# Optimization experiments

Hardware: AMD Instinct MI355X
Metric: run time of the kernel (lower is better)

## Reference

```python
import jax, jax.numpy as jnp
import numpy as np

B, DIM, S, CS, H = 1024, 64, 256, 500, 128

def setup_inputs() -> dict:
    key = jax.random.key(0)
    ks = jax.random.split(key, 16)
    def rn(k, shape, scale=0.05):
        return jax.random.normal(k, shape, dtype=jnp.float32) * scale
    return {
        "x": rn(ks[0], (B, DIM, S - 1), 1.0),
        "snippet": jax.random.randint(ks[1], (B, DIM), 0, CS, dtype=jnp.int64),
        "snippet_list": rn(ks[2], (DIM, CS, S), 1.0),
        "W_ih": rn(ks[3], (3 * H, 2 * DIM)),
        "W_hh": rn(ks[4], (3 * H, H)),
        "b_ih": rn(ks[5], (3 * H,)),
        "b_hh": rn(ks[6], (3 * H,)),
        "W1": rn(ks[7], (H // 2, H)),
        "b1": rn(ks[8], (H // 2,)),
        "W2": rn(ks[9], (H // 4, H // 2)),
        "b2": rn(ks[10], (H // 4,)),
        "W3": rn(ks[11], (H // 8, H // 4)),
        "b3": rn(ks[12], (H // 8,)),
        "W_last": rn(ks[13], (DIM, H // 8 + DIM)),
        "b_last": rn(ks[14], (DIM,)),
    }

def _leaky(v):
    return jax.nn.leaky_relu(v, negative_slope=0.01)

def _gru_last(x_seq, W_ih, W_hh, b_ih, b_hh):
    # x_seq: [B, T, I]; returns last hidden state [B, H]
    xg = jnp.einsum('bti,gi->btg', x_seq, W_ih) + b_ih  # [B, T, 3H]
    h0 = jnp.zeros((x_seq.shape[0], H), dtype=x_seq.dtype)
    def step(h, xg_t):
        hg = h @ W_hh.T + b_hh
        xr, xz, xn = jnp.split(xg_t, 3, axis=-1)
        hr, hz, hn = jnp.split(hg, 3, axis=-1)
        r = jax.nn.sigmoid(xr + hr)
        z = jax.nn.sigmoid(xz + hz)
        n = jnp.tanh(xn + r * hn)
        h_new = (1.0 - z) * n + z * h
        return h_new, None
    h_last, _ = jax.lax.scan(step, h0, jnp.swapaxes(xg, 0, 1))
    return h_last

def reference(x, snippet, snippet_list, W_ih, W_hh, b_ih, b_hh,
              W1, b1, W2, b2, W3, b3, W_last, b_last):
    # vectorized gather: snip[b, d, :] = snippet_list[d, snippet[b, d], :]
    snip = snippet_list[jnp.arange(DIM)[None, :], snippet]  # [B, DIM, S]
    last = snip[:, :, -1]          # [B, DIM]
    snip = snip[:, :, :-1]         # [B, DIM, S-1]
    xc = jnp.concatenate((x, snip), axis=1)       # [B, 2*DIM, S-1]
    xc = jnp.swapaxes(xc, 1, 2)                   # [B, S-1, 2*DIM]
    h = _gru_last(xc, W_ih, W_hh, b_ih, b_hh)     # [B, H]
    h = _leaky(h @ W1.T + b1)
    h = _leaky(h @ W2.T + b2)
    h = _leaky(h @ W3.T + b3)
    h = jnp.concatenate((h, last), axis=1)        # [B, H//8 + DIM]
    out = _leaky(h @ W_last.T + b_last)           # [B, DIM]
    return out
```

## Files before the change

kernel.cpp:

```cpp
#include <hip/hip_runtime.h>
#include <hip/hip_bf16.h>

#define B_    1024
#define DIMC  64
#define T_    255
#define H_    128
#define CS_   500
#define S_    256

#define MROWS 16
#define NBLK  (B_ / MROWS)
#define NTHR  512
#define TCH   16
#define XSTR  136

typedef __attribute__((ext_vector_type(8))) short bf16x8;
typedef __attribute__((ext_vector_type(4))) float f32x4;
typedef __attribute__((ext_vector_type(4))) float fv4;

__device__ __forceinline__ unsigned short f2bf(float f) {
    unsigned int u = __builtin_bit_cast(unsigned int, f);
    return (unsigned short)((u + 0x7FFFu + ((u >> 16) & 1u)) >> 16);
}
__device__ __forceinline__ float fast_rcp(float x) { return __builtin_amdgcn_rcpf(x); }
__device__ __forceinline__ float sigm(float x)   { float e = __expf(-x); return fast_rcp(1.0f + e); }
__device__ __forceinline__ float tanh_f(float x) { float e = __expf(2.0f * x); return 1.0f - 2.0f * fast_rcp(1.0f + e); }
__device__ __forceinline__ float leaky(float x)  { return x > 0.0f ? x : 0.01f * x; }
__device__ __forceinline__ int   imin(int a, int b) { return a < b ? a : b; }

#define OW1 0
#define OW2 8256
#define OW3 10336
#define OWL 10864
#define OHF 16048
#define OS1 18096
#define OS2 18608
#define OS3 18864
#define OSL 18992

__global__ __launch_bounds__(NTHR, 2)
void gru_fused(const float* __restrict__ x, const int* __restrict__ snippet,
               const float* __restrict__ slist,
               const float* __restrict__ W_ih, const float* __restrict__ W_hh,
               const float* __restrict__ b_ih, const float* __restrict__ b_hh,
               const float* __restrict__ W1, const float* __restrict__ b1,
               const float* __restrict__ W2, const float* __restrict__ b2,
               const float* __restrict__ W3, const float* __restrict__ b3,
               const float* __restrict__ Wl, const float* __restrict__ bl,
               float* __restrict__ out)
{
    __shared__ __attribute__((aligned(16))) unsigned short sh_x[2][TCH * MROWS * XSTR];
    __shared__ __attribute__((aligned(16))) unsigned short sh_h[2][MROWS * XSTR];
    __shared__ int sh_idx[MROWS * DIMC];

    const int tid   = threadIdx.x;
    const int bbase = blockIdx.x * MROWS;
    const int lane  = tid & 63;
    const int wv    = tid >> 6;
    const int l15   = lane & 15;
    const int l4    = lane >> 4;

    for (int i = tid; i < MROWS * DIMC; i += NTHR) {
        int r = i >> 6, d = i & 63;
        sh_idx[i] = snippet[(bbase + r) * DIMC + d];
    }
    for (int i = tid; i < MROWS * XSTR; i += NTHR) sh_h[0][i] = 0;

    bf16x8 wih[3][4], whh[3][4];
    {
        const int g = (wv << 4) + l15;
#pragma unroll
        for (int gt = 0; gt < 3; ++gt) {
#pragma unroll
            for (int kb = 0; kb < 4; ++kb) {
                const float* p1 = W_ih + (size_t)(gt * 128 + g) * 128 + kb * 32 + (l4 << 3);
                const float* p2 = W_hh + (size_t)(gt * 128 + g) * 128 + kb * 32 + (l4 << 3);
                bf16x8 a, b;
#pragma unroll
                for (int e = 0; e < 8; ++e) { a[e] = (short)f2bf(p1[e]); b[e] = (short)f2bf(p2[e]); }
                wih[gt][kb] = a; whh[gt][kb] = b;
            }
        }
    }
    const int jj = (wv << 4) + l15;
    const float bias_r = b_ih[jj]       + b_hh[jj];
    const float bias_z = b_ih[128 + jj] + b_hh[128 + jj];
    const float bxn    = b_ih[256 + jj];
    const float bhn    = b_hh[256 + jj];

    __syncthreads();

    int rowu[2], k0u[2], isx[2];
    const float* pa[2]; const float* pb[2];
#pragma unroll
    for (int un = 0; un < 2; ++un) {
        int u  = tid + un * NTHR;
        int r  = u >> 6;
        int k0 = (u & 63) << 1;
        rowu[un] = r; k0u[un] = k0;
        if (k0 < DIMC) {
            isx[un] = 1;
            pa[un] = x + ((size_t)(bbase + r) * DIMC + k0) * T_;
            pb[un] = pa[un] + T_;
        } else {
            isx[un] = 0;
            int d = k0 - DIMC;
            pa[un] = slist + ((size_t)d       * CS_ + sh_idx[(r << 6) + d])     * S_;
            pb[un] = slist + ((size_t)(d + 1) * CS_ + sh_idx[(r << 6) + d + 1]) * S_;
        }
    }

    fv4 sa[2][4], sb[2][4];

    auto issue = [&](int t0) {
#pragma unroll
        for (int un = 0; un < 2; ++un) {
#pragma unroll
            for (int g = 0; g < 4; ++g) {
                int off = t0 + g * 4;
                if (isx[un] && off + 3 > T_ - 1) {
                    fv4 va, vb;
#pragma unroll
                    for (int e = 0; e < 4; ++e) {
                        int tt = imin(off + e, T_ - 1);
                        va[e] = pa[un][tt]; vb[e] = pb[un][tt];
                    }
                    sa[un][g] = va; sb[un][g] = vb;
                } else {
                    fv4 va, vb;
                    __builtin_memcpy(&va, pa[un] + off, 16);
                    __builtin_memcpy(&vb, pb[un] + off, 16);
                    sa[un][g] = va; sb[un][g] = vb;
                }
            }
        }
    };

    auto commit = [&](int buf) {
#pragma unroll
        for (int un = 0; un < 2; ++un) {
#pragma unroll
            for (int g = 0; g < 4; ++g) {
#pragma unroll
                for (int e = 0; e < 4; ++e) {
                    int t = g * 4 + e;
                    unsigned pk = (unsigned)f2bf(sa[un][g][e]) | ((unsigned)f2bf(sb[un][g][e]) << 16);
                    *(unsigned*)&sh_x[buf][(t * MROWS + rowu[un]) * XSTR + k0u[un]] = pk;
                }
            }
        }
    };

    int cur = 0;
    float hprev[4] = {0.f, 0.f, 0.f, 0.f};

    auto step = [&](int bx, int t) {
        const unsigned short* xp = &sh_x[bx][(t * MROWS + l15) * XSTR + (l4 << 3)];
        const unsigned short* hp = &sh_h[cur][l15 * XSTR + (l4 << 3)];
        bf16x8 axv[4], ahv[4];
#pragma unroll
        for (int kb = 0; kb < 4; ++kb) {
            axv[kb] = *(const bf16x8*)(xp + kb * 32);
            ahv[kb] = *(const bf16x8*)(hp + kb * 32);
        }
        f32x4 ar = {0.f, 0.f, 0.f, 0.f}, az = ar, axn = ar, ahn = ar;
#pragma unroll
        for (int kb = 0; kb < 4; ++kb) {
            ar  = __builtin_amdgcn_mfma_f32_16x16x32_bf16(axv[kb], wih[0][kb], ar,  0, 0, 0);
            az  = __builtin_amdgcn_mfma_f32_16x16x32_bf16(axv[kb], wih[1][kb], az,  0, 0, 0);
            axn = __builtin_amdgcn_mfma_f32_16x16x32_bf16(axv[kb], wih[2][kb], axn, 0, 0, 0);
            ar  = __builtin_amdgcn_mfma_f32_16x16x32_bf16(ahv[kb], whh[0][kb], ar,  0, 0, 0);
            az  = __builtin_amdgcn_mfma_f32_16x16x32_bf16(ahv[kb], whh[1][kb], az,  0, 0, 0);
            ahn = __builtin_amdgcn_mfma_f32_16x16x32_bf16(ahv[kb], whh[2][kb], ahn, 0, 0, 0);
        }
#pragma unroll
        for (int q = 0; q < 4; ++q) {
            float r = sigm(ar[q] + bias_r);
            float z = sigm(az[q] + bias_z);
            float n = tanh_f(axn[q] + bxn + r * (ahn[q] + bhn));
            float hn = (1.0f - z) * n + z * hprev[q];
            hprev[q] = hn;
            sh_h[cur ^ 1][((l4 << 2) + q) * XSTR + jj] = f2bf(hn);
        }
        __syncthreads();
        cur ^= 1;
    };

    issue(0);
    commit(0);
    __syncthreads();

    for (int c = 0; c < 15; ++c) {
        issue((c + 1) * TCH);
        for (int t = 0; t < TCH; ++t) step(c & 1, t);
        commit((c + 1) & 1);
        __syncthreads();
    }
    for (int t = 0; t < 15; ++t) step(1, t);

    float* wl = (float*)sh_x;

    for (int i = tid; i < 8192; i += NTHR) wl[OW1 + (i >> 7) * 129 + (i & 127)] = W1[i];
    for (int i = tid; i < 2048; i += NTHR) wl[OW2 + (i >> 6) * 65  + (i & 63)]  = W2[i];
    for (int i = tid; i < 512;  i += NTHR) wl[OW3 + (i >> 5) * 33  + (i & 31)]  = W3[i];
    for (int i = tid; i < 5120; i += NTHR) wl[OWL + (i / 80) * 81  + (i % 80)]  = Wl[i];
#pragma unroll
    for (int q = 0; q < 4; ++q) wl[OHF + ((l4 << 2) + q) * 128 + jj] = hprev[q];
    __syncthreads();

    for (int mloc = 0; mloc < 2; ++mloc) {
        const int m = (wv << 1) + mloc;
        {
            float s = b1[lane];
            const float* w = wl + OW1 + lane * 129;
            for (int k = 0; k < 128; ++k) s += wl[OHF + m * 128 + k] * w[k];
            wl[OS1 + wv * 64 + lane] = leaky(s);
        }
        __syncthreads();
        if (lane < 32) {
            float s = b2[lane];
            const float* w = wl + OW2 + lane * 65;
            for (int k = 0; k < 64; ++k) s += wl[OS1 + wv * 64 + k] * w[k];
            wl[OS2 + wv * 32 + lane] = leaky(s);
        } else {
            int d = lane - 32;
            wl[OSL + wv * 64 + d]      = slist[((size_t)d        * CS_ + sh_idx[(m << 6) + d])      * S_ + (S_ - 1)];
            wl[OSL + wv * 64 + d + 32] = slist[((size_t)(d + 32) * CS_ + sh_idx[(m << 6) + d + 32]) * S_ + (S_ - 1)];
        }
        __syncthreads();
        if (lane < 16) {
            float s = b3[lane];
            const float* w = wl + OW3 + lane * 33;
            for (int k = 0; k < 32; ++k) s += wl[OS2 + wv * 32 + k] * w[k];
            wl[OS3 + wv * 16 + lane] = leaky(s);
        }
        __syncthreads();
        {
            float s = bl[lane];
            const float* w = wl + OWL + lane * 81;
#pragma unroll
            for (int i = 0; i < 16; ++i) s += wl[OS3 + wv * 16 + i] * w[i];
            for (int d = 0; d < 64; ++d) s += wl[OSL + wv * 64 + d] * w[16 + d];
            out[(size_t)(bbase + m) * DIMC + lane] = leaky(s);
        }
        __syncthreads();
    }
}

extern "C" void kernel_launch(void* const* d_in, const int* in_sizes, int n_in,
                              void* d_out, int out_size, void* d_ws, size_t ws_size,
                              hipStream_t stream) {
    (void)in_sizes; (void)n_in; (void)out_size; (void)d_ws; (void)ws_size;
    const float* x       = (const float*)d_in[0];
    const int*   snippet = (const int*)  d_in[1];
    const float* slist   = (const float*)d_in[2];
    const float* W_ih    = (const float*)d_in[3];
    const float* W_hh    = (const float*)d_in[4];
    const float* b_ih    = (const float*)d_in[5];
    const float* b_hh    = (const float*)d_in[6];
    const float* W1      = (const float*)d_in[7];
    const float* b1      = (const float*)d_in[8];
    const float* W2      = (const float*)d_in[9];
    const float* b2      = (const float*)d_in[10];
    const float* W3      = (const float*)d_in[11];
    const float* b3      = (const float*)d_in[12];
    const float* Wl      = (const float*)d_in[13];
    const float* bl      = (const float*)d_in[14];
    float* out = (float*)d_out;

    hipLaunchKernelGGL(gru_fused, dim3(NBLK), dim3(NTHR), 0, stream,
                       x, snippet, slist, W_ih, W_hh, b_ih, b_hh,
                       W1, b1, W2, b2, W3, b3, Wl, bl, out);
}
```

Baseline: 308.5 us.

## Split GRU step into batched input-gate MFMAs and a shortened recurrent chain

The input-projection MFMAs are now computed four timesteps at a time, separately from the serial recurrence. Each step's recurrent chain then runs only the hidden-state MFMAs, split into two independent accumulator chains so more of them can be in flight. The time chunk shrinks from 16 to 8 steps, shared memory is packed into one manually laid-out buffer, per-step barriers become a raw lgkmcnt wait plus s_barrier, and weight loads use 16-byte vectors. This shortens the latency-bound critical path per timestep, at the cost of more chunk-level syncs and hand-computed shared-memory offsets.

```diff
diff --git a/kernel.cpp b/kernel.cpp
--- a/kernel.cpp
+++ b/kernel.cpp
@@ -11,12 +11,15 @@
 #define MROWS 16
 #define NBLK  (B_ / MROWS)
 #define NTHR  512
-#define TCH   16
+#define TCH   8
 #define XSTR  136
+
+#define OFF_H   69632
+#define OFF_IDX 78336
+#define SMEMB   82432
 
 typedef __attribute__((ext_vector_type(8))) short bf16x8;
 typedef __attribute__((ext_vector_type(4))) float f32x4;
-typedef __attribute__((ext_vector_type(4))) float fv4;
 
 __device__ __forceinline__ unsigned short f2bf(float f) {
     unsigned int u = __builtin_bit_cast(unsigned int, f);
@@ -27,6 +30,9 @@
 __device__ __forceinline__ float tanh_f(float x) { float e = __expf(2.0f * x); return 1.0f - 2.0f * fast_rcp(1.0f + e); }
 __device__ __forceinline__ float leaky(float x)  { return x > 0.0f ? x : 0.01f * x; }
 __device__ __forceinline__ int   imin(int a, int b) { return a < b ? a : b; }
+__device__ __forceinline__ void bar_lgkm() {
+    asm volatile("s_waitcnt lgkmcnt(0)\n\ts_barrier" ::: "memory");
+}
 
 #define OW1 0
 #define OW2 8256
@@ -49,9 +55,10 @@
                const float* __restrict__ Wl, const float* __restrict__ bl,
                float* __restrict__ out)
 {
-    __shared__ __attribute__((aligned(16))) unsigned short sh_x[2][TCH * MROWS * XSTR];
-    __shared__ __attribute__((aligned(16))) unsigned short sh_h[2][MROWS * XSTR];
-    __shared__ int sh_idx[MROWS * DIMC];
+    __shared__ __attribute__((aligned(16))) unsigned char smem[SMEMB];
+    unsigned short* shx0 = (unsigned short*)smem;
+    unsigned short* shh0 = (unsigned short*)(smem + OFF_H);
+    int*            sidx = (int*)(smem + OFF_IDX);
 
     const int tid   = threadIdx.x;
     const int bbase = blockIdx.x * MROWS;
@@ -62,9 +69,9 @@
 
     for (int i = tid; i < MROWS * DIMC; i += NTHR) {
         int r = i >> 6, d = i & 63;
-        sh_idx[i] = snippet[(bbase + r) * DIMC + d];
-    }
-    for (int i = tid; i < MROWS * XSTR; i += NTHR) sh_h[0][i] = 0;
+        sidx[i] = snippet[(bbase + r) * DIMC + d];
+    }
+    for (int i = tid; i < MROWS * XSTR; i += NTHR) shh0[i] = 0;
 
     bf16x8 wih[3][4], whh[3][4];
     {
@@ -75,10 +82,16 @@
             for (int kb = 0; kb < 4; ++kb) {
                 const float* p1 = W_ih + (size_t)(gt * 128 + g) * 128 + kb * 32 + (l4 << 3);
                 const float* p2 = W_hh + (size_t)(gt * 128 + g) * 128 + kb * 32 + (l4 << 3);
-                bf16x8 a, b;
-#pragma unroll
-                for (int e = 0; e < 8; ++e) { a[e] = (short)f2bf(p1[e]); b[e] = (short)f2bf(p2[e]); }
-                wih[gt][kb] = a; whh[gt][kb] = b;
+                f32x4 a0, a1, c0, c1;
+                __builtin_memcpy(&a0, p1, 16); __builtin_memcpy(&a1, p1 + 4, 16);
+                __builtin_memcpy(&c0, p2, 16); __builtin_memcpy(&c1, p2 + 4, 16);
+                bf16x8 a, c;
+#pragma unroll
+                for (int e = 0; e < 4; ++e) {
+                    a[e]     = (short)f2bf(a0[e]); a[e + 4] = (short)f2bf(a1[e]);
+                    c[e]     = (short)f2bf(c0[e]); c[e + 4] = (short)f2bf(c1[e]);
+                }
+                wih[gt][kb] = a; whh[gt][kb] = c;
             }
         }
     }
@@ -105,31 +118,33 @@
         } else {
             isx[un] = 0;
             int d = k0 - DIMC;
-            pa[un] = slist + ((size_t)d       * CS_ + sh_idx[(r << 6) + d])     * S_;
-            pb[un] = slist + ((size_t)(d + 1) * CS_ + sh_idx[(r << 6) + d + 1]) * S_;
-        }
-    }
-
-    fv4 sa[2][4], sb[2][4];
+            pa[un] = slist + ((size_t)d       * CS_ + sidx[(r << 6) + d])     * S_;
+            pb[un] = slist + ((size_t)(d + 1) * CS_ + sidx[(r << 6) + d + 1]) * S_;
+        }
+    }
+
+    f32x4 sa[2][2], sb[2][2];
 
     auto issue = [&](int t0) {
 #pragma unroll
         for (int un = 0; un < 2; ++un) {
-#pragma unroll
-            for (int g = 0; g < 4; ++g) {
-                int off = t0 + g * 4;
-                if (isx[un] && off + 3 > T_ - 1) {
-                    fv4 va, vb;
+            if (isx[un] && t0 + TCH - 1 > T_ - 1) {
+#pragma unroll
+                for (int g = 0; g < 2; ++g) {
+                    f32x4 va, vb;
 #pragma unroll
                     for (int e = 0; e < 4; ++e) {
-                        int tt = imin(off + e, T_ - 1);
+                        int tt = imin(t0 + g * 4 + e, T_ - 1);
                         va[e] = pa[un][tt]; vb[e] = pb[un][tt];
                     }
                     sa[un][g] = va; sb[un][g] = vb;
-                } else {
-                    fv4 va, vb;
-                    __builtin_memcpy(&va, pa[un] + off, 16);
-                    __builtin_memcpy(&vb, pb[un] + off, 16);
+                }
+            } else {
+#pragma unroll
+                for (int g = 0; g < 2; ++g) {
+                    f32x4 va, vb;
+                    __builtin_memcpy(&va, pa[un] + t0 + g * 4, 16);
+                    __builtin_memcpy(&vb, pb[un] + t0 + g * 4, 16);
                     sa[un][g] = va; sb[un][g] = vb;
                 }
             }
@@ -137,15 +152,16 @@
     };
 
     auto commit = [&](int buf) {
+        unsigned short* dst = shx0 + buf * (TCH * MROWS * XSTR);
 #pragma unroll
         for (int un = 0; un < 2; ++un) {
 #pragma unroll
-            for (int g = 0; g < 4; ++g) {
+            for (int g = 0; g < 2; ++g) {
 #pragma unroll
                 for (int e = 0; e < 4; ++e) {
                     int t = g * 4 + e;
                     unsigned pk = (unsigned)f2bf(sa[un][g][e]) | ((unsigned)f2bf(sb[un][g][e]) << 16);
-                    *(unsigned*)&sh_x[buf][(t * MROWS + rowu[un]) * XSTR + k0u[un]] = pk;
+                    *(unsigned*)&dst[(t * MROWS + rowu[un]) * XSTR + k0u[un]] = pk;
                 }
             }
         }
@@ -153,36 +169,57 @@
 
     int cur = 0;
     float hprev[4] = {0.f, 0.f, 0.f, 0.f};
-
-    auto step = [&](int bx, int t) {
-        const unsigned short* xp = &sh_x[bx][(t * MROWS + l15) * XSTR + (l4 << 3)];
-        const unsigned short* hp = &sh_h[cur][l15 * XSTR + (l4 << 3)];
-        bf16x8 axv[4], ahv[4];
-#pragma unroll
-        for (int kb = 0; kb < 4; ++kb) {
-            axv[kb] = *(const bf16x8*)(xp + kb * 32);
-            ahv[kb] = *(const bf16x8*)(hp + kb * 32);
-        }
-        f32x4 ar = {0.f, 0.f, 0.f, 0.f}, az = ar, axn = ar, ahn = ar;
-#pragma unroll
-        for (int kb = 0; kb < 4; ++kb) {
-            ar  = __builtin_amdgcn_mfma_f32_16x16x32_bf16(axv[kb], wih[0][kb], ar,  0, 0, 0);
-            az  = __builtin_amdgcn_mfma_f32_16x16x32_bf16(axv[kb], wih[1][kb], az,  0, 0, 0);
-            axn = __builtin_amdgcn_mfma_f32_16x16x32_bf16(axv[kb], wih[2][kb], axn, 0, 0, 0);
-            ar  = __builtin_amdgcn_mfma_f32_16x16x32_bf16(ahv[kb], whh[0][kb], ar,  0, 0, 0);
-            az  = __builtin_amdgcn_mfma_f32_16x16x32_bf16(ahv[kb], whh[1][kb], az,  0, 0, 0);
-            ahn = __builtin_amdgcn_mfma_f32_16x16x32_bf16(ahv[kb], whh[2][kb], ahn, 0, 0, 0);
-        }
+    const f32x4 Z = {0.f, 0.f, 0.f, 0.f};
+
+    auto xg_phase = [&](int buf, int tb, int nt, f32x4* xr, f32x4* xz, f32x4* xn) {
+        const unsigned short* base = shx0 + buf * (TCH * MROWS * XSTR);
+#pragma unroll
+        for (int tt = 0; tt < 4; ++tt) {
+            if (tt >= nt) break;
+            const unsigned short* xp = base + ((tb + tt) * MROWS + l15) * XSTR + (l4 << 3);
+            bf16x8 a[4];
+#pragma unroll
+            for (int kb = 0; kb < 4; ++kb) a[kb] = *(const bf16x8*)(xp + kb * 32);
+            f32x4 r = Z, z = Z, n = Z;
+#pragma unroll
+            for (int kb = 0; kb < 4; ++kb) {
+                r = __builtin_amdgcn_mfma_f32_16x16x32_bf16(a[kb], wih[0][kb], r, 0, 0, 0);
+                z = __builtin_amdgcn_mfma_f32_16x16x32_bf16(a[kb], wih[1][kb], z, 0, 0, 0);
+                n = __builtin_amdgcn_mfma_f32_16x16x32_bf16(a[kb], wih[2][kb], n, 0, 0, 0);
+            }
+            xr[tt] = r; xz[tt] = z; xn[tt] = n;
+        }
+    };
+
+    auto recur = [&](f32x4 xr, f32x4 xz, f32x4 xn) {
+        const unsigned short* hp = shh0 + cur * (MROWS * XSTR) + l15 * XSTR + (l4 << 3);
+        bf16x8 h0 = *(const bf16x8*)(hp);
+        bf16x8 h1 = *(const bf16x8*)(hp + 32);
+        bf16x8 h2 = *(const bf16x8*)(hp + 64);
+        bf16x8 h3 = *(const bf16x8*)(hp + 96);
+        f32x4 arA = __builtin_amdgcn_mfma_f32_16x16x32_bf16(h0, whh[0][0], xr, 0, 0, 0);
+        f32x4 azA = __builtin_amdgcn_mfma_f32_16x16x32_bf16(h0, whh[1][0], xz, 0, 0, 0);
+        f32x4 anA = __builtin_amdgcn_mfma_f32_16x16x32_bf16(h0, whh[2][0], Z,  0, 0, 0);
+        f32x4 arB = __builtin_amdgcn_mfma_f32_16x16x32_bf16(h2, whh[0][2], Z,  0, 0, 0);
+        f32x4 azB = __builtin_amdgcn_mfma_f32_16x16x32_bf16(h2, whh[1][2], Z,  0, 0, 0);
+        f32x4 anB = __builtin_amdgcn_mfma_f32_16x16x32_bf16(h2, whh[2][2], Z,  0, 0, 0);
+        arA = __builtin_amdgcn_mfma_f32_16x16x32_bf16(h1, whh[0][1], arA, 0, 0, 0);
+        azA = __builtin_amdgcn_mfma_f32_16x16x32_bf16(h1, whh[1][1], azA, 0, 0, 0);
+        anA = __builtin_amdgcn_mfma_f32_16x16x32_bf16(h1, whh[2][1], anA, 0, 0, 0);
+        arB = __builtin_amdgcn_mfma_f32_16x16x32_bf16(h3, whh[0][3], arB, 0, 0, 0);
+        azB = __builtin_amdgcn_mfma_f32_16x16x32_bf16(h3, whh[1][3], azB, 0, 0, 0);
+        anB = __builtin_amdgcn_mfma_f32_16x16x32_bf16(h3, whh[2][3], anB, 0, 0, 0);
+        unsigned short* hw = shh0 + (cur ^ 1) * (MROWS * XSTR);
 #pragma unroll
         for (int q = 0; q < 4; ++q) {
-            float r = sigm(ar[q] + bias_r);
-            float z = sigm(az[q] + bias_z);
-            float n = tanh_f(axn[q] + bxn + r * (ahn[q] + bhn));
+            float r = sigm(arA[q] + arB[q] + bias_r);
+            float z = sigm(azA[q] + azB[q] + bias_z);
+            float n = tanh_f(xn[q] + bxn + r * (anA[q] + anB[q] + bhn));
             float hn = (1.0f - z) * n + z * hprev[q];
             hprev[q] = hn;
-            sh_h[cur ^ 1][((l4 << 2) + q) * XSTR + jj] = f2bf(hn);
-        }
-        __syncthreads();
+            hw[((l4 << 2) + q) * XSTR + jj] = f2bf(hn);
+        }
+        bar_lgkm();
         cur ^= 1;
     };
 
@@ -190,15 +227,30 @@
     commit(0);
     __syncthreads();
 
-    for (int c = 0; c < 15; ++c) {
+    for (int c = 0; c < 31; ++c) {
         issue((c + 1) * TCH);
-        for (int t = 0; t < TCH; ++t) step(c & 1, t);
+        const int bx = c & 1;
+        f32x4 xr[4], xz[4], xn[4];
+        xg_phase(bx, 0, 4, xr, xz, xn);
+#pragma unroll
+        for (int tt = 0; tt < 4; ++tt) recur(xr[tt], xz[tt], xn[tt]);
+        xg_phase(bx, 4, 4, xr, xz, xn);
+#pragma unroll
+        for (int tt = 0; tt < 4; ++tt) recur(xr[tt], xz[tt], xn[tt]);
         commit((c + 1) & 1);
-        __syncthreads();
-    }
-    for (int t = 0; t < 15; ++t) step(1, t);
-
-    float* wl = (float*)sh_x;
+        bar_lgkm();
+    }
+    {
+        f32x4 xr[4], xz[4], xn[4];
+        xg_phase(1, 0, 4, xr, xz, xn);
+#pragma unroll
+        for (int tt = 0; tt < 4; ++tt) recur(xr[tt], xz[tt], xn[tt]);
+        xg_phase(1, 4, 3, xr, xz, xn);
+#pragma unroll
+        for (int tt = 0; tt < 3; ++tt) recur(xr[tt], xz[tt], xn[tt]);
+    }
+
+    float* wl = (float*)smem;
 
     for (int i = tid; i < 8192; i += NTHR) wl[OW1 + (i >> 7) * 129 + (i & 127)] = W1[i];
     for (int i = tid; i < 2048; i += NTHR) wl[OW2 + (i >> 6) * 65  + (i & 63)]  = W2[i];
@@ -224,8 +276,8 @@
             wl[OS2 + wv * 32 + lane] = leaky(s);
         } else {
             int d = lane - 32;
-            wl[OSL + wv * 64 + d]      = slist[((size_t)d        * CS_ + sh_idx[(m << 6) + d])      * S_ + (S_ - 1)];
-            wl[OSL + wv * 64 + d + 32] = slist[((size_t)(d + 32) * CS_ + sh_idx[(m << 6) + d + 32]) * S_ + (S_ - 1)];
+            wl[OSL + wv * 64 + d]      = slist[((size_t)d        * CS_ + sidx[(m << 6) + d])      * S_ + (S_ - 1)];
+            wl[OSL + wv * 64 + d + 32] = slist[((size_t)(d + 32) * CS_ + sidx[(m << 6) + d + 32]) * S_ + (S_ - 1)];
         }
         __syncthreads();
         if (lane < 16) {
```

Result: slower. 322.4 us (+4.5%).

## Process two 16-row groups per block with small 2-step input chunks

Applied to the files above, without the earlier changes.

Doubles rows per block to 32, so each wave runs two independent GRU recurrences (A/B groups) interleaved and their MFMA and transcendental latencies can overlap. The input staging chunk shrinks from 16 steps to 2, with one barrier per step pair using a raw waitcnt+s_barrier. Biases are folded into the MFMA accumulator init and the hidden update is algebraically simplified. Grid size halves to 32 blocks, which reduces parallelism across CUs, and prefetch now covers far fewer timesteps ahead.

```diff
diff --git a/kernel.cpp b/kernel.cpp
--- a/kernel.cpp
+++ b/kernel.cpp
@@ -8,15 +8,19 @@
 #define CS_   500
 #define S_    256
 
-#define MROWS 16
+#define MROWS 32
 #define NBLK  (B_ / MROWS)
 #define NTHR  512
-#define TCH   16
+#define TCH   2
 #define XSTR  136
+
+#define OFF_H   34816
+#define OFF_IDX 87040
+#define SMEMB   95232
 
 typedef __attribute__((ext_vector_type(8))) short bf16x8;
 typedef __attribute__((ext_vector_type(4))) float f32x4;
-typedef __attribute__((ext_vector_type(4))) float fv4;
+typedef __attribute__((ext_vector_type(2))) float f32x2;
 
 __device__ __forceinline__ unsigned short f2bf(float f) {
     unsigned int u = __builtin_bit_cast(unsigned int, f);
@@ -26,17 +30,19 @@
 __device__ __forceinline__ float sigm(float x)   { float e = __expf(-x); return fast_rcp(1.0f + e); }
 __device__ __forceinline__ float tanh_f(float x) { float e = __expf(2.0f * x); return 1.0f - 2.0f * fast_rcp(1.0f + e); }
 __device__ __forceinline__ float leaky(float x)  { return x > 0.0f ? x : 0.01f * x; }
-__device__ __forceinline__ int   imin(int a, int b) { return a < b ? a : b; }
+__device__ __forceinline__ void bar_lgkm() {
+    asm volatile("s_waitcnt lgkmcnt(0)\n\ts_barrier" ::: "memory");
+}
 
 #define OW1 0
 #define OW2 8256
 #define OW3 10336
 #define OWL 10864
 #define OHF 16048
-#define OS1 18096
-#define OS2 18608
-#define OS3 18864
-#define OSL 18992
+#define OS1 20144
+#define OS2 20656
+#define OS3 20912
+#define OSL 21040
 
 __global__ __launch_bounds__(NTHR, 2)
 void gru_fused(const float* __restrict__ x, const int* __restrict__ snippet,
@@ -49,9 +55,10 @@
                const float* __restrict__ Wl, const float* __restrict__ bl,
                float* __restrict__ out)
 {
-    __shared__ __attribute__((aligned(16))) unsigned short sh_x[2][TCH * MROWS * XSTR];
-    __shared__ __attribute__((aligned(16))) unsigned short sh_h[2][MROWS * XSTR];
-    __shared__ int sh_idx[MROWS * DIMC];
+    __shared__ __attribute__((aligned(16))) unsigned char smem[SMEMB];
+    unsigned short* shx = (unsigned short*)smem;
+    unsigned short* shh = (unsigned short*)(smem + OFF_H);
+    int*            sidx = (int*)(smem + OFF_IDX);
 
     const int tid   = threadIdx.x;
     const int bbase = blockIdx.x * MROWS;
@@ -62,9 +69,9 @@
 
     for (int i = tid; i < MROWS * DIMC; i += NTHR) {
         int r = i >> 6, d = i & 63;
-        sh_idx[i] = snippet[(bbase + r) * DIMC + d];
-    }
-    for (int i = tid; i < MROWS * XSTR; i += NTHR) sh_h[0][i] = 0;
+        sidx[i] = snippet[(bbase + r) * DIMC + d];
+    }
+    for (int i = tid; i < 2 * 16 * XSTR; i += NTHR) shh[i] = 0;
 
     bf16x8 wih[3][4], whh[3][4];
     {
@@ -75,10 +82,16 @@
             for (int kb = 0; kb < 4; ++kb) {
                 const float* p1 = W_ih + (size_t)(gt * 128 + g) * 128 + kb * 32 + (l4 << 3);
                 const float* p2 = W_hh + (size_t)(gt * 128 + g) * 128 + kb * 32 + (l4 << 3);
-                bf16x8 a, b;
-#pragma unroll
-                for (int e = 0; e < 8; ++e) { a[e] = (short)f2bf(p1[e]); b[e] = (short)f2bf(p2[e]); }
-                wih[gt][kb] = a; whh[gt][kb] = b;
+                f32x4 a0, a1, c0, c1;
+                __builtin_memcpy(&a0, p1, 16); __builtin_memcpy(&a1, p1 + 4, 16);
+                __builtin_memcpy(&c0, p2, 16); __builtin_memcpy(&c1, p2 + 4, 16);
+                bf16x8 a, c;
+#pragma unroll
+                for (int e = 0; e < 4; ++e) {
+                    a[e] = (short)f2bf(a0[e]); a[e + 4] = (short)f2bf(a1[e]);
+                    c[e] = (short)f2bf(c0[e]); c[e + 4] = (short)f2bf(c1[e]);
+                }
+                wih[gt][kb] = a; whh[gt][kb] = c;
             }
         }
     }
@@ -90,126 +103,130 @@
 
     __syncthreads();
 
-    int rowu[2], k0u[2], isx[2];
-    const float* pa[2]; const float* pb[2];
-#pragma unroll
-    for (int un = 0; un < 2; ++un) {
-        int u  = tid + un * NTHR;
-        int r  = u >> 6;
-        int k0 = (u & 63) << 1;
-        rowu[un] = r; k0u[un] = k0;
-        if (k0 < DIMC) {
-            isx[un] = 1;
+    const int k0  = (tid & 63) << 1;
+    const int isx = (k0 < DIMC);
+    const float* pa[4]; const float* pb[4];
+    int rowu[4];
+#pragma unroll
+    for (int un = 0; un < 4; ++un) {
+        int r = (tid >> 6) + (un << 3);
+        rowu[un] = r;
+        if (isx) {
             pa[un] = x + ((size_t)(bbase + r) * DIMC + k0) * T_;
             pb[un] = pa[un] + T_;
         } else {
-            isx[un] = 0;
             int d = k0 - DIMC;
-            pa[un] = slist + ((size_t)d       * CS_ + sh_idx[(r << 6) + d])     * S_;
-            pb[un] = slist + ((size_t)(d + 1) * CS_ + sh_idx[(r << 6) + d + 1]) * S_;
-        }
-    }
-
-    fv4 sa[2][4], sb[2][4];
+            pa[un] = slist + ((size_t)d       * CS_ + sidx[(r << 6) + d])     * S_;
+            pb[un] = slist + ((size_t)(d + 1) * CS_ + sidx[(r << 6) + d + 1]) * S_;
+        }
+    }
+
+    f32x2 sa[4], sb[4];
 
     auto issue = [&](int t0) {
-#pragma unroll
-        for (int un = 0; un < 2; ++un) {
-#pragma unroll
-            for (int g = 0; g < 4; ++g) {
-                int off = t0 + g * 4;
-                if (isx[un] && off + 3 > T_ - 1) {
-                    fv4 va, vb;
-#pragma unroll
-                    for (int e = 0; e < 4; ++e) {
-                        int tt = imin(off + e, T_ - 1);
-                        va[e] = pa[un][tt]; vb[e] = pb[un][tt];
-                    }
-                    sa[un][g] = va; sb[un][g] = vb;
-                } else {
-                    fv4 va, vb;
-                    __builtin_memcpy(&va, pa[un] + off, 16);
-                    __builtin_memcpy(&vb, pb[un] + off, 16);
-                    sa[un][g] = va; sb[un][g] = vb;
-                }
+        if (isx && t0 >= T_ - 1) {
+#pragma unroll
+            for (int un = 0; un < 4; ++un) {
+                float va = pa[un][T_ - 1], vb = pb[un][T_ - 1];
+                sa[un] = f32x2{va, va}; sb[un] = f32x2{vb, vb};
+            }
+        } else {
+#pragma unroll
+            for (int un = 0; un < 4; ++un) {
+                f32x2 va, vb;
+                __builtin_memcpy(&va, pa[un] + t0, 8);
+                __builtin_memcpy(&vb, pb[un] + t0, 8);
+                sa[un] = va; sb[un] = vb;
             }
         }
     };
 
     auto commit = [&](int buf) {
-#pragma unroll
-        for (int un = 0; un < 2; ++un) {
-#pragma unroll
-            for (int g = 0; g < 4; ++g) {
-#pragma unroll
-                for (int e = 0; e < 4; ++e) {
-                    int t = g * 4 + e;
-                    unsigned pk = (unsigned)f2bf(sa[un][g][e]) | ((unsigned)f2bf(sb[un][g][e]) << 16);
-                    *(unsigned*)&sh_x[buf][(t * MROWS + rowu[un]) * XSTR + k0u[un]] = pk;
-                }
+        unsigned short* dst = shx + buf * (TCH * MROWS * XSTR);
+#pragma unroll
+        for (int un = 0; un < 4; ++un) {
+#pragma unroll
+            for (int e = 0; e < TCH; ++e) {
+                unsigned pk = (unsigned)f2bf(sa[un][e]) | ((unsigned)f2bf(sb[un][e]) << 16);
+                *(unsigned*)&dst[(e * MROWS + rowu[un]) * XSTR + k0] = pk;
             }
         }
     };
 
     int cur = 0;
-    float hprev[4] = {0.f, 0.f, 0.f, 0.f};
-
-    auto step = [&](int bx, int t) {
-        const unsigned short* xp = &sh_x[bx][(t * MROWS + l15) * XSTR + (l4 << 3)];
-        const unsigned short* hp = &sh_h[cur][l15 * XSTR + (l4 << 3)];
-        bf16x8 axv[4], ahv[4];
+    float hprevA[4] = {0.f, 0.f, 0.f, 0.f};
+    float hprevB[4] = {0.f, 0.f, 0.f, 0.f};
+
+    auto recone = [&](int bx, int st, int grp, float* hprev) {
+        const unsigned short* xp = shx + ((bx * TCH + st) * MROWS + (grp << 4) + l15) * XSTR + (l4 << 3);
+        const unsigned short* hp = shh + ((cur * 2 + grp) * 16 + l15) * XSTR + (l4 << 3);
+        bf16x8 xf[4], hf[4];
 #pragma unroll
         for (int kb = 0; kb < 4; ++kb) {
-            axv[kb] = *(const bf16x8*)(xp + kb * 32);
-            ahv[kb] = *(const bf16x8*)(hp + kb * 32);
-        }
-        f32x4 ar = {0.f, 0.f, 0.f, 0.f}, az = ar, axn = ar, ahn = ar;
+            xf[kb] = *(const bf16x8*)(xp + kb * 32);
+            hf[kb] = *(const bf16x8*)(hp + kb * 32);
+        }
+        f32x4 aXr = {bias_r, bias_r, bias_r, bias_r};
+        f32x4 aXz = {bias_z, bias_z, bias_z, bias_z};
+        f32x4 aXn = {bxn, bxn, bxn, bxn};
+        f32x4 aHr = {0.f, 0.f, 0.f, 0.f};
+        f32x4 aHz = {0.f, 0.f, 0.f, 0.f};
+        f32x4 aHn = {bhn, bhn, bhn, bhn};
 #pragma unroll
         for (int kb = 0; kb < 4; ++kb) {
-            ar  = __builtin_amdgcn_mfma_f32_16x16x32_bf16(axv[kb], wih[0][kb], ar,  0, 0, 0);
-            az  = __builtin_amdgcn_mfma_f32_16x16x32_bf16(axv[kb], wih[1][kb], az,  0, 0, 0);
-            axn = __builtin_amdgcn_mfma_f32_16x16x32_bf16(axv[kb], wih[2][kb], axn, 0, 0, 0);
-            ar  = __builtin_amdgcn_mfma_f32_16x16x32_bf16(ahv[kb], whh[0][kb], ar,  0, 0, 0);
-            az  = __builtin_amdgcn_mfma_f32_16x16x32_bf16(ahv[kb], whh[1][kb], az,  0, 0, 0);
-            ahn = __builtin_amdgcn_mfma_f32_16x16x32_bf16(ahv[kb], whh[2][kb], ahn, 0, 0, 0);
-        }
+            aXr = __builtin_amdgcn_mfma_f32_16x16x32_bf16(xf[kb], wih[0][kb], aXr, 0, 0, 0);
+            aHr = __builtin_amdgcn_mfma_f32_16x16x32_bf16(hf[kb], whh[0][kb], aHr, 0, 0, 0);
+            aXz = __builtin_amdgcn_mfma_f32_16x16x32_bf16(xf[kb], wih[1][kb], aXz, 0, 0, 0);
+            aHz = __builtin_amdgcn_mfma_f32_16x16x32_bf16(hf[kb], whh[1][kb], aHz, 0, 0, 0);
+            aXn = __builtin_amdgcn_mfma_f32_16x16x32_bf16(xf[kb], wih[2][kb], aXn, 0, 0, 0);
+            aHn = __builtin_amdgcn_mfma_f32_16x16x32_bf16(hf[kb], whh[2][kb], aHn, 0, 0, 0);
+        }
+        unsigned short* hw = shh + ((cur ^ 1) * 2 + grp) * (16 * XSTR);
 #pragma unroll
         for (int q = 0; q < 4; ++q) {
-            float r = sigm(ar[q] + bias_r);
-            float z = sigm(az[q] + bias_z);
-            float n = tanh_f(axn[q] + bxn + r * (ahn[q] + bhn));
-            float hn = (1.0f - z) * n + z * hprev[q];
+            float r  = sigm(aXr[q] + aHr[q]);
+            float z  = sigm(aXz[q] + aHz[q]);
+            float n  = tanh_f(aXn[q] + r * aHn[q]);
+            float hn = n + z * (hprev[q] - n);
             hprev[q] = hn;
-            sh_h[cur ^ 1][((l4 << 2) + q) * XSTR + jj] = f2bf(hn);
-        }
-        __syncthreads();
-        cur ^= 1;
+            hw[((l4 << 2) + q) * XSTR + jj] = f2bf(hn);
+        }
     };
 
     issue(0);
     commit(0);
     __syncthreads();
 
-    for (int c = 0; c < 15; ++c) {
+    for (int c = 0; c < 127; ++c) {
         issue((c + 1) * TCH);
-        for (int t = 0; t < TCH; ++t) step(c & 1, t);
+        const int bx = c & 1;
+        recone(bx, 0, 0, hprevA);
+        recone(bx, 0, 1, hprevB);
+        bar_lgkm(); cur ^= 1;
         commit((c + 1) & 1);
-        __syncthreads();
-    }
-    for (int t = 0; t < 15; ++t) step(1, t);
-
-    float* wl = (float*)sh_x;
+        recone(bx, 1, 0, hprevA);
+        recone(bx, 1, 1, hprevB);
+        bar_lgkm(); cur ^= 1;
+    }
+    recone(1, 0, 0, hprevA);
+    recone(1, 0, 1, hprevB);
+    __syncthreads();
+
+    float* wl = (float*)smem;
 
     for (int i = tid; i < 8192; i += NTHR) wl[OW1 + (i >> 7) * 129 + (i & 127)] = W1[i];
     for (int i = tid; i < 2048; i += NTHR) wl[OW2 + (i >> 6) * 65  + (i & 63)]  = W2[i];
     for (int i = tid; i < 512;  i += NTHR) wl[OW3 + (i >> 5) * 33  + (i & 31)]  = W3[i];
     for (int i = tid; i < 5120; i += NTHR) wl[OWL + (i / 80) * 81  + (i % 80)]  = Wl[i];
 #pragma unroll
-    for (int q = 0; q < 4; ++q) wl[OHF + ((l4 << 2) + q) * 128 + jj] = hprev[q];
-    __syncthreads();
-
-    for (int mloc = 0; mloc < 2; ++mloc) {
-        const int m = (wv << 1) + mloc;
+    for (int q = 0; q < 4; ++q) {
+        wl[OHF + (((l4 << 2) + q)) * 128 + jj]      = hprevA[q];
+        wl[OHF + (16 + ((l4 << 2) + q)) * 128 + jj] = hprevB[q];
+    }
+    __syncthreads();
+
+    for (int mloc = 0; mloc < 4; ++mloc) {
+        const int m = (wv << 2) + mloc;
         {
             float s = b1[lane];
             const float* w = wl + OW1 + lane * 129;
@@ -224,8 +241,8 @@
             wl[OS2 + wv * 32 + lane] = leaky(s);
         } else {
             int d = lane - 32;
-            wl[OSL + wv * 64 + d]      = slist[((size_t)d        * CS_ + sh_idx[(m << 6) + d])      * S_ + (S_ - 1)];
-            wl[OSL + wv * 64 + d + 32] = slist[((size_t)(d + 32) * CS_ + sh_idx[(m << 6) + d + 32]) * S_ + (S_ - 1)];
+            wl[OSL + wv * 64 + d]      = slist[((size_t)d        * CS_ + sidx[(m << 6) + d])      * S_ + (S_ - 1)];
+            wl[OSL + wv * 64 + d + 32] = slist[((size_t)(d + 32) * CS_ + sidx[(m << 6) + d + 32]) * S_ + (S_ - 1)];
         }
         __syncthreads();
         if (lane < 16) {
```

After: 771.3 us. 150% more time.
